# Kernel optimization log

Hardware: AMD Instinct MI355X
Metric: run time of the kernel (lower is better)

Reference implementation:

```python
import jax, jax.numpy as jnp
import numpy as np

D = 1024
H = 16
DH = D // H  # 64
FF_H = 4096
EPS = 1e-5


def layernorm(x, gamma, beta):
    mu = jnp.mean(x, axis=-1, keepdims=True)
    var = jnp.var(x, axis=-1, keepdims=True)
    return (x - mu) * jax.lax.rsqrt(var + EPS) * gamma + beta


def setup_inputs() -> dict:
    key = jax.random.key(0)
    ks = jax.random.split(key, 12)
    B, S = 2, 2048
    q = jax.random.normal(ks[0], (B, S, D), dtype=jnp.float32)
    k = jax.random.normal(ks[1], (B, S, D), dtype=jnp.float32)
    v = jax.random.normal(ks[2], (B, S, D), dtype=jnp.float32)
    time_lengths = jax.random.randint(ks[3], (B,), 0, S)
    mask = jnp.zeros((1, 1, S, S), dtype=jnp.float32)
    sc = 0.02
    Wq = jax.random.normal(ks[4], (D, D), dtype=jnp.float32) * sc
    Wk = jax.random.normal(ks[5], (D, D), dtype=jnp.float32) * sc
    Wv = jax.random.normal(ks[6], (D, D), dtype=jnp.float32) * sc
    Wd = jax.random.normal(ks[7], (D, D), dtype=jnp.float32) * sc
    W1 = jax.random.normal(ks[8], (D, FF_H), dtype=jnp.float32) * sc
    b1 = jnp.zeros((FF_H,), dtype=jnp.float32)
    W2 = jax.random.normal(ks[9], (FF_H, D), dtype=jnp.float32) * sc
    b2 = jnp.zeros((D,), dtype=jnp.float32)
    g1 = jnp.ones((D,), dtype=jnp.float32)
    be1 = jnp.zeros((D,), dtype=jnp.float32)
    g2 = jnp.ones((D,), dtype=jnp.float32)
    be2 = jnp.zeros((D,), dtype=jnp.float32)
    return {"q": q, "k": k, "v": v, "time_lengths": time_lengths, "mask": mask,
            "Wq": Wq, "Wk": Wk, "Wv": Wv, "Wd": Wd,
            "W1": W1, "b1": b1, "W2": W2, "b2": b2,
            "g1": g1, "be1": be1, "g2": g2, "be2": be2}


def reference(q, k, v, time_lengths, mask, Wq, Wk, Wv, Wd, W1, b1, W2, b2, g1, be1, g2, be2):
    B, S, _ = q.shape
    scale = jnp.sqrt(jnp.float32(DH))
    # project and split heads: [B,H,S,DH]
    qh = (q @ Wq).reshape(B, S, H, DH).transpose(0, 2, 1, 3)
    kh = (k @ Wk).reshape(B, S, H, DH).transpose(0, 2, 1, 3)
    vh = (v @ Wv).reshape(B, S, H, DH).transpose(0, 2, 1, 3)
    score = jnp.einsum('bhqd,bhkd->bhqk', qh, kh) / scale + mask
    attn = jax.nn.softmax(score, axis=-1)
    z = jnp.einsum('bhqk,bhkd->bhqd', attn, vh)
    z = z.transpose(0, 2, 1, 3).reshape(B, S, D)
    z = z @ Wd
    # Add & LayerNorm 1 (note: original applies LN to attn out, then adds q)
    x = layernorm(z, g1, be1) + q
    # FF (dropout is identity in eval)
    ff = jax.nn.relu(x @ W1 + b1) @ W2 + b2
    return layernorm(ff + x, g2, be2)
```

## Files before the change

### kernel.cpp

```cpp
#include <hip/hip_runtime.h>
#include <hip/hip_bf16.h>


#define SEQ 2048
#define DM  1024
#define LNEPS 1e-5f

typedef __attribute__((ext_vector_type(8))) short bf16x8;
typedef __attribute__((ext_vector_type(4))) float f32x4;

#define GAS __attribute__((address_space(1)))
#define LAS __attribute__((address_space(3)))

static __device__ __forceinline__ void gl_lds16(const unsigned short* g, unsigned short* l) {
    __builtin_amdgcn_global_load_lds((const GAS void*)g, (LAS void*)l, 16, 0, 0);
}

static __device__ __forceinline__ unsigned short f2bf(float f) {
    unsigned u = __builtin_bit_cast(unsigned, f);
    u += 0x7fffu + ((u >> 16) & 1u);
    return (unsigned short)(u >> 16);
}

__global__ __launch_bounds__(256) void gemm_bf16(
    const unsigned short* __restrict__ A, const unsigned short* __restrict__ Bt,
    float* __restrict__ Cf, unsigned short* __restrict__ Cb,
    int M, int N, int Klen, int lda, int ldb,
    size_t sA, size_t sB, size_t sC,
    const float* __restrict__ bias, int ep)
{
    __shared__ unsigned short As[128 * 32];
    __shared__ unsigned short Bs[128 * 32];

    const int t = threadIdx.x, lane = t & 63, w = t >> 6;
    const int wm = w >> 1, wn = w & 1;
    const int m0 = blockIdx.y * 128, n0 = blockIdx.x * 128;
    A  += (size_t)blockIdx.z * sA;
    Bt += (size_t)blockIdx.z * sB;
    const size_t cbase = (size_t)blockIdx.z * sC;
    const int l15 = lane & 15, l16 = lane >> 4;
    const int ar = lane >> 2, ac = (lane & 3) * 8;

    f32x4 acc[4][4];
    #pragma unroll
    for (int i = 0; i < 4; i++)
        #pragma unroll
        for (int j = 0; j < 4; j++)
            acc[i][j] = (f32x4){0.f, 0.f, 0.f, 0.f};

    for (int k0 = 0; k0 < Klen; k0 += 32) {
        __syncthreads();
        #pragma unroll
        for (int i = 0; i < 2; i++) {
            const int rg = w * 2 + i;
            gl_lds16(&A [(size_t)(m0 + rg * 16 + ar) * lda + k0 + ac], &As[rg * 512]);
            gl_lds16(&Bt[(size_t)(n0 + rg * 16 + ar) * ldb + k0 + ac], &Bs[rg * 512]);
        }
        __syncthreads();

        bf16x8 af[4], bfr[4];
        #pragma unroll
        for (int i = 0; i < 4; i++) {
            af[i]  = *(const bf16x8*)&As[(wm * 64 + i * 16 + l15) * 32 + l16 * 8];
            bfr[i] = *(const bf16x8*)&Bs[(wn * 64 + i * 16 + l15) * 32 + l16 * 8];
        }
        #pragma unroll
        for (int mi = 0; mi < 4; mi++)
            #pragma unroll
            for (int ni = 0; ni < 4; ni++)
                acc[mi][ni] = __builtin_amdgcn_mfma_f32_16x16x32_bf16(
                    af[mi], bfr[ni], acc[mi][ni], 0, 0, 0);
    }

    #pragma unroll
    for (int ni = 0; ni < 4; ni++) {
        const int col = n0 + wn * 64 + ni * 16 + l15;
        const float bv = (ep && blockIdx.z == 0) ? bias[col] : 0.f;
        #pragma unroll
        for (int mi = 0; mi < 4; mi++) {
            #pragma unroll
            for (int r = 0; r < 4; r++) {
                const int row = m0 + wm * 64 + mi * 16 + l16 * 4 + r;
                float vv = acc[mi][ni][r] + bv;
                if (ep == 2) vv = fmaxf(vv, 0.f);
                if (Cf) Cf[cbase + (size_t)row * N + col] = vv;
                else    Cb[cbase + (size_t)row * N + col] = f2bf(vv);
            }
        }
    }
}

__global__ __launch_bounds__(256) void attn_mfma(
    const unsigned short* __restrict__ qh, const unsigned short* __restrict__ kh,
    const unsigned short* __restrict__ vhT, const float* __restrict__ mask,
    unsigned short* __restrict__ z)
{
    __shared__ unsigned short Ks0[64 * 64];
    __shared__ unsigned short Ks1[64 * 64];
    __shared__ unsigned short Vst[64 * 64];
    __shared__ unsigned short Ps[64 * 72];

    const int t = threadIdx.x, lane = t & 63, w = t >> 6;
    const int bid = blockIdx.x;
    const int qt = bid >> 5, h = bid & 15, b = (bid >> 4) & 1;
    const int q0 = qt * 64, qr = w * 16;
    const int l15 = lane & 15, l16 = lane >> 4;

    const int lr = lane >> 3;
    const int gc = ((lane & 7) ^ lr) * 8;

    const size_t qbase = (size_t)(b * SEQ + q0) * DM + h * 64;
    const size_t kbase = (size_t)(b * SEQ) * DM + h * 64;
    const size_t vbase = (size_t)((b * 16 + h) * 64) * SEQ;

    #pragma unroll
    for (int i = 0; i < 2; i++) {
        const int rg = w * 2 + i;
        gl_lds16(&qh[qbase + (size_t)(rg * 8 + lr) * DM + gc], &Ks1[rg * 512]);
        gl_lds16(&kh[kbase + (size_t)(rg * 8 + lr) * DM + gc], &Ks0[rg * 512]);
    }
    __syncthreads();

    const int sw0 = ((l16    ) ^ (l15 & 7)) * 8;
    const int sw1 = ((l16 + 4) ^ (l15 & 7)) * 8;
    const bf16x8 bQ0 = *(const bf16x8*)&Ks1[(qr + l15) * 64 + sw0];
    const bf16x8 bQ1 = *(const bf16x8*)&Ks1[(qr + l15) * 64 + sw1];
    __syncthreads();

    const float* mrow = mask + (size_t)(q0 + qr + l15) * SEQ;

    float m_i = -1e30f, l_i = 0.f;
    f32x4 o4[4];
    #pragma unroll
    for (int mi = 0; mi < 4; mi++) o4[mi] = (f32x4){0.f, 0.f, 0.f, 0.f};

    for (int kt = 0; kt < SEQ / 64; kt++) {
        const int k0 = kt * 64;
        const int kn = ((kt + 1) & (SEQ / 64 - 1)) * 64;
        unsigned short* Kcur = (kt & 1) ? Ks1 : Ks0;
        unsigned short* Knxt = (kt & 1) ? Ks0 : Ks1;

        __builtin_amdgcn_s_barrier();

        float4 mv[4];
        #pragma unroll
        for (int ki = 0; ki < 4; ki++)
            mv[ki] = *(const float4*)&mrow[k0 + ki * 16 + l16 * 4];

        #pragma unroll
        for (int i = 0; i < 2; i++) {
            const int rg = w * 2 + i;
            gl_lds16(&vhT[vbase + (size_t)(rg * 8 + lr) * SEQ + k0 + gc], &Vst[rg * 512]);
        }
        __builtin_amdgcn_sched_barrier(0);
        #pragma unroll
        for (int i = 0; i < 2; i++) {
            const int rg = w * 2 + i;
            gl_lds16(&kh[kbase + (size_t)(kn + rg * 8 + lr) * DM + gc], &Knxt[rg * 512]);
        }

        asm volatile("s_waitcnt vmcnt(8)" ::: "memory");
        __builtin_amdgcn_s_barrier();
        __builtin_amdgcn_sched_barrier(0);

        f32x4 s4[4];
        __builtin_amdgcn_s_setprio(1);
        #pragma unroll
        for (int ki = 0; ki < 4; ki++) {
            const int r = ki * 16 + l15;
            const bf16x8 aK0 = *(const bf16x8*)&Kcur[r * 64 + sw0];
            const bf16x8 aK1 = *(const bf16x8*)&Kcur[r * 64 + sw1];
            f32x4 a0 = (f32x4){0.f, 0.f, 0.f, 0.f};
            a0 = __builtin_amdgcn_mfma_f32_16x16x32_bf16(aK0, bQ0, a0, 0, 0, 0);
            s4[ki] = __builtin_amdgcn_mfma_f32_16x16x32_bf16(aK1, bQ1, a0, 0, 0, 0);
        }
        __builtin_amdgcn_s_setprio(0);

        float sv[4][4];
        #pragma unroll
        for (int ki = 0; ki < 4; ki++) {
            sv[ki][0] = s4[ki][0] * 0.125f + mv[ki].x;
            sv[ki][1] = s4[ki][1] * 0.125f + mv[ki].y;
            sv[ki][2] = s4[ki][2] * 0.125f + mv[ki].z;
            sv[ki][3] = s4[ki][3] * 0.125f + mv[ki].w;
        }

        float rm = -1e30f;
        #pragma unroll
        for (int ki = 0; ki < 4; ki++)
            #pragma unroll
            for (int r = 0; r < 4; r++) rm = fmaxf(rm, sv[ki][r]);
        rm = fmaxf(rm, __shfl_xor(rm, 16));
        rm = fmaxf(rm, __shfl_xor(rm, 32));
        const float mnew  = fmaxf(m_i, rm);
        const float alpha = __expf(m_i - mnew);
        m_i = mnew;

        float ps = 0.f;
        #pragma unroll
        for (int ki = 0; ki < 4; ki++) {
            float p[4];
            #pragma unroll
            for (int r = 0; r < 4; r++) { p[r] = __expf(sv[ki][r] - mnew); ps += p[r]; }
            ushort4 pk;
            pk.x = f2bf(p[0]); pk.y = f2bf(p[1]); pk.z = f2bf(p[2]); pk.w = f2bf(p[3]);
            *(ushort4*)&Ps[(qr + l15) * 72 + ki * 16 + l16 * 4] = pk;
        }
        ps += __shfl_xor(ps, 16);
        ps += __shfl_xor(ps, 32);
        l_i = l_i * alpha + ps;
        #pragma unroll
        for (int mi = 0; mi < 4; mi++)
            #pragma unroll
            for (int r = 0; r < 4; r++) o4[mi][r] *= alpha;

        asm volatile("s_waitcnt vmcnt(2)" ::: "memory");
        __builtin_amdgcn_s_barrier();
        __builtin_amdgcn_sched_barrier(0);

        const bf16x8 bP0 = *(const bf16x8*)&Ps[(qr + l15) * 72 + l16 * 8];
        const bf16x8 bP1 = *(const bf16x8*)&Ps[(qr + l15) * 72 + 32 + l16 * 8];
        __builtin_amdgcn_s_setprio(1);
        #pragma unroll
        for (int mi = 0; mi < 4; mi++) {
            const int r = mi * 16 + l15;
            const bf16x8 aV0 = *(const bf16x8*)&Vst[r * 64 + sw0];
            const bf16x8 aV1 = *(const bf16x8*)&Vst[r * 64 + sw1];
            o4[mi] = __builtin_amdgcn_mfma_f32_16x16x32_bf16(aV0, bP0, o4[mi], 0, 0, 0);
            o4[mi] = __builtin_amdgcn_mfma_f32_16x16x32_bf16(aV1, bP1, o4[mi], 0, 0, 0);
        }
        __builtin_amdgcn_s_setprio(0);
    }

    asm volatile("s_waitcnt vmcnt(0)" ::: "memory");

    const float inv = 1.f / l_i;
    #pragma unroll
    for (int mi = 0; mi < 4; mi++) {
        ushort4 ok;
        ok.x = f2bf(o4[mi][0] * inv); ok.y = f2bf(o4[mi][1] * inv);
        ok.z = f2bf(o4[mi][2] * inv); ok.w = f2bf(o4[mi][3] * inv);
        *(ushort4*)&z[(size_t)(b * SEQ + q0 + qr + l15) * DM + h * 64 + mi * 16 + l16 * 4] = ok;
    }
}

__global__ __launch_bounds__(256) void cast3_bf16(
    const float* __restrict__ a0, const float* __restrict__ a1, const float* __restrict__ a2,
    unsigned short* __restrict__ out)
{
    const float* src = blockIdx.z == 0 ? a0 : (blockIdx.z == 1 ? a1 : a2);
    const size_t i = ((size_t)blockIdx.x * 256 + threadIdx.x) * 4;
    const float4 v = *(const float4*)&src[i];
    ushort4 o; o.x = f2bf(v.x); o.y = f2bf(v.y); o.z = f2bf(v.z); o.w = f2bf(v.w);
    *(ushort4*)&out[(size_t)blockIdx.z * ((size_t)SEQ * 2 * DM) + i] = o;
}

__global__ __launch_bounds__(256) void transpose_cast(
    const float* __restrict__ W, unsigned short* __restrict__ Wt, int K, int N)
{
    __shared__ float ts[64][65];
    const int n0 = blockIdx.x * 64, k0 = blockIdx.y * 64;
    const int t = threadIdx.x, r = t >> 4, c4 = (t & 15) * 4;
    #pragma unroll
    for (int i = 0; i < 4; i++) {
        const float4 v = *(const float4*)&W[(size_t)(k0 + r + i * 16) * N + n0 + c4];
        ts[r + i * 16][c4 + 0] = v.x; ts[r + i * 16][c4 + 1] = v.y;
        ts[r + i * 16][c4 + 2] = v.z; ts[r + i * 16][c4 + 3] = v.w;
    }
    __syncthreads();
    #pragma unroll
    for (int i = 0; i < 4; i++) {
        const int n = r + i * 16;
        ushort4 o;
        o.x = f2bf(ts[c4 + 0][n]); o.y = f2bf(ts[c4 + 1][n]);
        o.z = f2bf(ts[c4 + 2][n]); o.w = f2bf(ts[c4 + 3][n]);
        *(ushort4*)&Wt[(size_t)(n0 + n) * K + k0 + c4] = o;
    }
}

__global__ __launch_bounds__(256) void transpose_v(
    const unsigned short* __restrict__ vh, unsigned short* __restrict__ vhT)
{
    __shared__ unsigned short ts[64][80];
    const int s0 = blockIdx.x * 64, h = blockIdx.y, b = blockIdx.z;
    const int t = threadIdx.x, rr = t >> 3, c8 = (t & 7) * 8;
    #pragma unroll
    for (int i = 0; i < 2; i++) {
        const int srow = rr + i * 32;
        *(uint4*)&ts[srow][c8] = *(const uint4*)&vh[(size_t)(b * SEQ + s0 + srow) * DM + h * 64 + c8];
    }
    __syncthreads();
    #pragma unroll
    for (int i = 0; i < 2; i++) {
        const int dr = rr + i * 32;
        ushort4 ov0, ov1;
        ov0.x = ts[c8 + 0][dr]; ov0.y = ts[c8 + 1][dr];
        ov0.z = ts[c8 + 2][dr]; ov0.w = ts[c8 + 3][dr];
        ov1.x = ts[c8 + 4][dr]; ov1.y = ts[c8 + 5][dr];
        ov1.z = ts[c8 + 6][dr]; ov1.w = ts[c8 + 7][dr];
        *(ushort4*)&vhT[(size_t)((b * 16 + h) * 64 + dr) * SEQ + s0 + c8] = ov0;
        *(ushort4*)&vhT[(size_t)((b * 16 + h) * 64 + dr) * SEQ + s0 + c8 + 4] = ov1;
    }
}

__global__ __launch_bounds__(256) void ln_res(
    const float* __restrict__ a, const float* __restrict__ a2,
    const float* __restrict__ r,
    const float* __restrict__ g, const float* __restrict__ be,
    float* __restrict__ out, unsigned short* __restrict__ outb, int mode)
{
    __shared__ float redls[8];
    const int row = blockIdx.x, t = threadIdx.x;
    const size_t base = (size_t)row * DM;

    float vals[4], s = 0.f, sq = 0.f;
    #pragma unroll
    for (int i = 0; i < 4; i++) {
        const int c = t + 256 * i;
        float x = a[base + c];
        if (a2) x += a2[base + c];
        if (mode == 1) x += r[base + c];
        vals[i] = x; s += x; sq += x * x;
    }
    #pragma unroll
    for (int off = 32; off > 0; off >>= 1) { s += __shfl_down(s, off); sq += __shfl_down(sq, off); }
    if ((t & 63) == 0) { redls[t >> 6] = s; redls[4 + (t >> 6)] = sq; }
    __syncthreads();
    s  = redls[0] + redls[1] + redls[2] + redls[3];
    sq = redls[4] + redls[5] + redls[6] + redls[7];

    const float mu  = s * (1.f / 1024.f);
    const float var = sq * (1.f / 1024.f) - mu * mu;
    const float rs  = rsqrtf(var + LNEPS);
    #pragma unroll
    for (int i = 0; i < 4; i++) {
        const int c = t + 256 * i;
        float y = (vals[i] - mu) * rs * g[c] + be[c];
        if (mode == 0) y += r[base + c];
        out[base + c] = y;
        if (outb) outb[base + c] = f2bf(y);
    }
}

extern "C" void kernel_launch(void* const* d_in, const int* in_sizes, int n_in,
                              void* d_out, int out_size, void* d_ws, size_t ws_size,
                              hipStream_t stream)
{
    const float* q    = (const float*)d_in[0];
    const float* k    = (const float*)d_in[1];
    const float* v    = (const float*)d_in[2];
    const float* mask = (const float*)d_in[4];
    const float* Wq   = (const float*)d_in[5];
    const float* Wk   = (const float*)d_in[6];
    const float* Wv   = (const float*)d_in[7];
    const float* Wd   = (const float*)d_in[8];
    const float* W1   = (const float*)d_in[9];
    const float* b1   = (const float*)d_in[10];
    const float* W2   = (const float*)d_in[11];
    const float* b2   = (const float*)d_in[12];
    const float* g1   = (const float*)d_in[13];
    const float* be1  = (const float*)d_in[14];
    const float* g2   = (const float*)d_in[15];
    const float* be2  = (const float*)d_in[16];
    float* out = (float*)d_out;

    char* WS = (char*)d_ws;
    const size_t MiB = 1u << 20;
    const size_t ND  = (size_t)4096 * 1024;

    unsigned short* qb  = (unsigned short*)(WS + 0);
    unsigned short* vhT = (unsigned short*)(WS + 0);
    unsigned short* zb  = (unsigned short*)(WS + 8 * MiB);
    unsigned short* xb  = (unsigned short*)(WS + 16 * MiB);
    unsigned short* Wqt = (unsigned short*)(WS + 24 * MiB);
    unsigned short* Wdt = (unsigned short*)(WS + 30 * MiB);
    unsigned short* W1t = (unsigned short*)(WS + 32 * MiB);
    unsigned short* W2t = (unsigned short*)(WS + 40 * MiB);
    unsigned short* qh  = (unsigned short*)(WS + 48 * MiB);
    float*          zd0 = (float*)(WS + 48 * MiB);
    float*          zd1 = (float*)(WS + 64 * MiB);
    float*          x   = (float*)(WS + 80 * MiB);
    unsigned short* h1  = (unsigned short*)(WS + 96 * MiB);
    float*          y0  = (float*)(WS + 48 * MiB);
    float*          y1  = (float*)(WS + 64 * MiB);

    unsigned short* kh = qh + ND;
    unsigned short* vh = qh + 2 * ND;

    const dim3 blk(256);

    cast3_bf16<<<dim3(4096, 1, 3), blk, 0, stream>>>(q, k, v, qb);
    transpose_cast<<<dim3(16, 16), blk, 0, stream>>>(Wq, Wqt,                   1024, 1024);
    transpose_cast<<<dim3(16, 16), blk, 0, stream>>>(Wk, Wqt + 1024 * 1024,     1024, 1024);
    transpose_cast<<<dim3(16, 16), blk, 0, stream>>>(Wv, Wqt + 2 * 1024 * 1024, 1024, 1024);
    transpose_cast<<<dim3(16, 16), blk, 0, stream>>>(Wd, Wdt, 1024, 1024);
    transpose_cast<<<dim3(64, 16), blk, 0, stream>>>(W1, W1t, 1024, 4096);
    transpose_cast<<<dim3(16, 64), blk, 0, stream>>>(W2, W2t, 4096, 1024);

    gemm_bf16<<<dim3(8, 32, 3), blk, 0, stream>>>(qb, Wqt, nullptr, qh,
        4096, 1024, 1024, 1024, 1024, ND, (size_t)1024 * 1024, ND, nullptr, 0);

    transpose_v<<<dim3(32, 16, 2), blk, 0, stream>>>(vh, vhT);

    attn_mfma<<<dim3(1024), blk, 0, stream>>>(qh, kh, vhT, mask, zb);

    gemm_bf16<<<dim3(8, 32, 2), blk, 0, stream>>>(zb, Wdt, zd0, nullptr,
        4096, 1024, 512, 1024, 1024, 512, 512, ND, nullptr, 0);

    ln_res<<<dim3(4096), blk, 0, stream>>>(zd0, zd1, q, g1, be1, x, xb, 0);

    gemm_bf16<<<dim3(32, 32, 1), blk, 0, stream>>>(xb, W1t, nullptr, h1,
        4096, 4096, 1024, 1024, 1024, 0, 0, 0, b1, 2);
    gemm_bf16<<<dim3(8, 32, 2), blk, 0, stream>>>(h1, W2t, y0, nullptr,
        4096, 1024, 2048, 4096, 4096, 2048, 2048, ND, b2, 1);

    ln_res<<<dim3(4096), blk, 0, stream>>>(y0, y1, x, g2, be2, out, nullptr, 1);
}
```

Before: 495.8 us.

## Double-buffer GEMM, fuse V transpose into epilogue, merge prep kernels, lazy softmax rescale

```diff
diff --git a/kernel.cpp b/kernel.cpp
--- a/kernel.cpp
+++ b/kernel.cpp
@@ -22,15 +22,22 @@
     return (unsigned short)(u >> 16);
 }
 
+static __device__ __forceinline__ unsigned cvt_pk_bf16(float lo, float hi) {
+    unsigned r;
+    asm("v_cvt_pk_bf16_f32 %0, %1, %2" : "=v"(r) : "v"(lo), "v"(hi));
+    return r;
+}
+
 __global__ __launch_bounds__(256) void gemm_bf16(
     const unsigned short* __restrict__ A, const unsigned short* __restrict__ Bt,
     float* __restrict__ Cf, unsigned short* __restrict__ Cb,
+    unsigned short* __restrict__ CbT,
     int M, int N, int Klen, int lda, int ldb,
     size_t sA, size_t sB, size_t sC,
     const float* __restrict__ bias, int ep)
 {
-    __shared__ unsigned short As[128 * 32];
-    __shared__ unsigned short Bs[128 * 32];
+    __shared__ unsigned short As[2][128 * 32];
+    __shared__ unsigned short Bs[2][128 * 32];
 
     const int t = threadIdx.x, lane = t & 63, w = t >> 6;
     const int wm = w >> 1, wn = w & 1;
@@ -48,21 +55,20 @@
         for (int j = 0; j < 4; j++)
             acc[i][j] = (f32x4){0.f, 0.f, 0.f, 0.f};
 
-    for (int k0 = 0; k0 < Klen; k0 += 32) {
-        __syncthreads();
+    auto stage = [&](int buf, int k0) {
         #pragma unroll
         for (int i = 0; i < 2; i++) {
             const int rg = w * 2 + i;
-            gl_lds16(&A [(size_t)(m0 + rg * 16 + ar) * lda + k0 + ac], &As[rg * 512]);
-            gl_lds16(&Bt[(size_t)(n0 + rg * 16 + ar) * ldb + k0 + ac], &Bs[rg * 512]);
-        }
-        __syncthreads();
-
+            gl_lds16(&A [(size_t)(m0 + rg * 16 + ar) * lda + k0 + ac], &As[buf][rg * 512]);
+            gl_lds16(&Bt[(size_t)(n0 + rg * 16 + ar) * ldb + k0 + ac], &Bs[buf][rg * 512]);
+        }
+    };
+    auto compute = [&](int buf) {
         bf16x8 af[4], bfr[4];
         #pragma unroll
         for (int i = 0; i < 4; i++) {
-            af[i]  = *(const bf16x8*)&As[(wm * 64 + i * 16 + l15) * 32 + l16 * 8];
-            bfr[i] = *(const bf16x8*)&Bs[(wn * 64 + i * 16 + l15) * 32 + l16 * 8];
+            af[i]  = *(const bf16x8*)&As[buf][(wm * 64 + i * 16 + l15) * 32 + l16 * 8];
+            bfr[i] = *(const bf16x8*)&Bs[buf][(wn * 64 + i * 16 + l15) * 32 + l16 * 8];
         }
         #pragma unroll
         for (int mi = 0; mi < 4; mi++)
@@ -70,6 +76,35 @@
             for (int ni = 0; ni < 4; ni++)
                 acc[mi][ni] = __builtin_amdgcn_mfma_f32_16x16x32_bf16(
                     af[mi], bfr[ni], acc[mi][ni], 0, 0, 0);
+    };
+
+    stage(0, 0);
+    __syncthreads();
+    int k0 = 0;
+    for (; k0 + 32 < Klen; k0 += 32) {
+        const int cur = (k0 >> 5) & 1;
+        stage(cur ^ 1, k0 + 32);
+        compute(cur);
+        __syncthreads();
+    }
+    compute((k0 >> 5) & 1);
+
+    if (CbT && blockIdx.z == 2) {
+        #pragma unroll
+        for (int ni = 0; ni < 4; ni++) {
+            const int col = n0 + wn * 64 + ni * 16 + l15;
+            const int hh = col >> 6, d = col & 63;
+            #pragma unroll
+            for (int mi = 0; mi < 4; mi++) {
+                const int row = m0 + wm * 64 + mi * 16 + l16 * 4;
+                const int bb = row >> 11, s = row & 2047;
+                ushort4 o;
+                o.x = f2bf(acc[mi][ni][0]); o.y = f2bf(acc[mi][ni][1]);
+                o.z = f2bf(acc[mi][ni][2]); o.w = f2bf(acc[mi][ni][3]);
+                *(ushort4*)&CbT[((size_t)((bb * 16 + hh) * 64 + d)) * SEQ + s] = o;
+            }
+        }
+        return;
     }
 
     #pragma unroll
@@ -176,43 +211,50 @@
         }
         __builtin_amdgcn_s_setprio(0);
 
-        float sv[4][4];
+        float sv[16];
         #pragma unroll
         for (int ki = 0; ki < 4; ki++) {
-            sv[ki][0] = s4[ki][0] * 0.125f + mv[ki].x;
-            sv[ki][1] = s4[ki][1] * 0.125f + mv[ki].y;
-            sv[ki][2] = s4[ki][2] * 0.125f + mv[ki].z;
-            sv[ki][3] = s4[ki][3] * 0.125f + mv[ki].w;
-        }
-
-        float rm = -1e30f;
-        #pragma unroll
-        for (int ki = 0; ki < 4; ki++)
-            #pragma unroll
-            for (int r = 0; r < 4; r++) rm = fmaxf(rm, sv[ki][r]);
+            sv[ki * 4 + 0] = s4[ki][0] * 0.125f + mv[ki].x;
+            sv[ki * 4 + 1] = s4[ki][1] * 0.125f + mv[ki].y;
+            sv[ki * 4 + 2] = s4[ki][2] * 0.125f + mv[ki].z;
+            sv[ki * 4 + 3] = s4[ki][3] * 0.125f + mv[ki].w;
+        }
+
+        float rm = fmaxf(sv[0], sv[1]);
+        #pragma unroll
+        for (int i = 2; i < 16; i += 2) rm = fmaxf(fmaxf(rm, sv[i]), sv[i + 1]);
         rm = fmaxf(rm, __shfl_xor(rm, 16));
         rm = fmaxf(rm, __shfl_xor(rm, 32));
-        const float mnew  = fmaxf(m_i, rm);
-        const float alpha = __expf(m_i - mnew);
-        m_i = mnew;
+
+        const bool skip = __all(rm <= m_i + 8.f);
+        float mnew = m_i, alpha = 1.f;
+        if (!skip) { mnew = fmaxf(m_i, rm); alpha = __expf(m_i - mnew); }
 
         float ps = 0.f;
         #pragma unroll
         for (int ki = 0; ki < 4; ki++) {
-            float p[4];
-            #pragma unroll
-            for (int r = 0; r < 4; r++) { p[r] = __expf(sv[ki][r] - mnew); ps += p[r]; }
-            ushort4 pk;
-            pk.x = f2bf(p[0]); pk.y = f2bf(p[1]); pk.z = f2bf(p[2]); pk.w = f2bf(p[3]);
-            *(ushort4*)&Ps[(qr + l15) * 72 + ki * 16 + l16 * 4] = pk;
+            const float p0 = __expf(sv[ki * 4 + 0] - mnew);
+            const float p1 = __expf(sv[ki * 4 + 1] - mnew);
+            const float p2 = __expf(sv[ki * 4 + 2] - mnew);
+            const float p3 = __expf(sv[ki * 4 + 3] - mnew);
+            ps += (p0 + p1) + (p2 + p3);
+            uint2 pk;
+            pk.x = cvt_pk_bf16(p0, p1);
+            pk.y = cvt_pk_bf16(p2, p3);
+            *(uint2*)&Ps[(qr + l15) * 72 + ki * 16 + l16 * 4] = pk;
         }
         ps += __shfl_xor(ps, 16);
         ps += __shfl_xor(ps, 32);
-        l_i = l_i * alpha + ps;
-        #pragma unroll
-        for (int mi = 0; mi < 4; mi++)
+        if (!skip) {
+            m_i = mnew;
+            l_i = l_i * alpha + ps;
             #pragma unroll
-            for (int r = 0; r < 4; r++) o4[mi][r] *= alpha;
+            for (int mi = 0; mi < 4; mi++)
+                #pragma unroll
+                for (int r = 0; r < 4; r++) o4[mi][r] *= alpha;
+        } else {
+            l_i += ps;
+        }
 
         asm volatile("s_waitcnt vmcnt(2)" ::: "memory");
         __builtin_amdgcn_s_barrier();
@@ -237,35 +279,63 @@
     const float inv = 1.f / l_i;
     #pragma unroll
     for (int mi = 0; mi < 4; mi++) {
-        ushort4 ok;
-        ok.x = f2bf(o4[mi][0] * inv); ok.y = f2bf(o4[mi][1] * inv);
-        ok.z = f2bf(o4[mi][2] * inv); ok.w = f2bf(o4[mi][3] * inv);
-        *(ushort4*)&z[(size_t)(b * SEQ + q0 + qr + l15) * DM + h * 64 + mi * 16 + l16 * 4] = ok;
-    }
-}
-
-__global__ __launch_bounds__(256) void cast3_bf16(
-    const float* __restrict__ a0, const float* __restrict__ a1, const float* __restrict__ a2,
-    unsigned short* __restrict__ out)
+        const float a0 = o4[mi][0] * inv, a1 = o4[mi][1] * inv;
+        const float a2 = o4[mi][2] * inv, a3 = o4[mi][3] * inv;
+        uint2 ov;
+        ov.x = cvt_pk_bf16(a0, a1);
+        ov.y = cvt_pk_bf16(a2, a3);
+        *(uint2*)&z[(size_t)(b * SEQ + q0 + qr + l15) * DM + h * 64 + mi * 16 + l16 * 4] = ov;
+    }
+}
+
+__global__ __launch_bounds__(256) void prep(
+    const float* __restrict__ q, const float* __restrict__ k, const float* __restrict__ v,
+    unsigned short* __restrict__ qb,
+    const float* __restrict__ Wq, const float* __restrict__ Wk,
+    const float* __restrict__ Wv, const float* __restrict__ Wd,
+    const float* __restrict__ W1, const float* __restrict__ W2,
+    unsigned short* __restrict__ Wqt, unsigned short* __restrict__ Wdt,
+    unsigned short* __restrict__ W1t, unsigned short* __restrict__ W2t)
 {
-    const float* src = blockIdx.z == 0 ? a0 : (blockIdx.z == 1 ? a1 : a2);
-    const size_t i = ((size_t)blockIdx.x * 256 + threadIdx.x) * 4;
-    const float4 v = *(const float4*)&src[i];
-    ushort4 o; o.x = f2bf(v.x); o.y = f2bf(v.y); o.z = f2bf(v.z); o.w = f2bf(v.w);
-    *(ushort4*)&out[(size_t)blockIdx.z * ((size_t)SEQ * 2 * DM) + i] = o;
-}
-
-__global__ __launch_bounds__(256) void transpose_cast(
-    const float* __restrict__ W, unsigned short* __restrict__ Wt, int K, int N)
-{
+    const int z = blockIdx.z, t = threadIdx.x;
+    const int flat = blockIdx.y * 64 + blockIdx.x;
+
+    if (z < 3) {
+        const float* src = z == 0 ? q : (z == 1 ? k : v);
+        unsigned short* dst = qb + (size_t)z * ((size_t)SEQ * 2 * DM);
+        const size_t base = (size_t)flat * 4096 + t * 4;
+        #pragma unroll
+        for (int i = 0; i < 4; i++) {
+            const float4 w4 = *(const float4*)&src[base + i * 1024];
+            ushort4 o; o.x = f2bf(w4.x); o.y = f2bf(w4.y); o.z = f2bf(w4.z); o.w = f2bf(w4.w);
+            *(ushort4*)&dst[base + i * 1024] = o;
+        }
+        return;
+    }
+
     __shared__ float ts[64][65];
-    const int n0 = blockIdx.x * 64, k0 = blockIdx.y * 64;
-    const int t = threadIdx.x, r = t >> 4, c4 = (t & 15) * 4;
+    const float* W; unsigned short* Wt; int K, N, n0, k0;
+    if (z < 7) {
+        if (flat >= 256) return;
+        W  = z == 3 ? Wq : z == 4 ? Wk : (z == 5 ? Wv : Wd);
+        Wt = z == 3 ? Wqt : z == 4 ? Wqt + 1024 * 1024
+           : z == 5 ? Wqt + 2 * 1024 * 1024 : Wdt;
+        K = 1024; N = 1024;
+        n0 = (flat & 15) * 64; k0 = (flat >> 4) * 64;
+    } else if (z == 7) {
+        W = W1; Wt = W1t; K = 1024; N = 4096;
+        n0 = blockIdx.x * 64; k0 = blockIdx.y * 64;
+    } else {
+        W = W2; Wt = W2t; K = 4096; N = 1024;
+        n0 = (flat & 15) * 64; k0 = (flat >> 4) * 64;
+    }
+
+    const int r = t >> 4, c4 = (t & 15) * 4;
     #pragma unroll
     for (int i = 0; i < 4; i++) {
-        const float4 v = *(const float4*)&W[(size_t)(k0 + r + i * 16) * N + n0 + c4];
-        ts[r + i * 16][c4 + 0] = v.x; ts[r + i * 16][c4 + 1] = v.y;
-        ts[r + i * 16][c4 + 2] = v.z; ts[r + i * 16][c4 + 3] = v.w;
+        const float4 v4 = *(const float4*)&W[(size_t)(k0 + r + i * 16) * N + n0 + c4];
+        ts[r + i * 16][c4 + 0] = v4.x; ts[r + i * 16][c4 + 1] = v4.y;
+        ts[r + i * 16][c4 + 2] = v4.z; ts[r + i * 16][c4 + 3] = v4.w;
     }
     __syncthreads();
     #pragma unroll
@@ -275,31 +345,6 @@
         o.x = f2bf(ts[c4 + 0][n]); o.y = f2bf(ts[c4 + 1][n]);
         o.z = f2bf(ts[c4 + 2][n]); o.w = f2bf(ts[c4 + 3][n]);
         *(ushort4*)&Wt[(size_t)(n0 + n) * K + k0 + c4] = o;
-    }
-}
-
-__global__ __launch_bounds__(256) void transpose_v(
-    const unsigned short* __restrict__ vh, unsigned short* __restrict__ vhT)
-{
-    __shared__ unsigned short ts[64][80];
-    const int s0 = blockIdx.x * 64, h = blockIdx.y, b = blockIdx.z;
-    const int t = threadIdx.x, rr = t >> 3, c8 = (t & 7) * 8;
-    #pragma unroll
-    for (int i = 0; i < 2; i++) {
-        const int srow = rr + i * 32;
-        *(uint4*)&ts[srow][c8] = *(const uint4*)&vh[(size_t)(b * SEQ + s0 + srow) * DM + h * 64 + c8];
-    }
-    __syncthreads();
-    #pragma unroll
-    for (int i = 0; i < 2; i++) {
-        const int dr = rr + i * 32;
-        ushort4 ov0, ov1;
-        ov0.x = ts[c8 + 0][dr]; ov0.y = ts[c8 + 1][dr];
-        ov0.z = ts[c8 + 2][dr]; ov0.w = ts[c8 + 3][dr];
-        ov1.x = ts[c8 + 4][dr]; ov1.y = ts[c8 + 5][dr];
-        ov1.z = ts[c8 + 6][dr]; ov1.w = ts[c8 + 7][dr];
-        *(ushort4*)&vhT[(size_t)((b * 16 + h) * 64 + dr) * SEQ + s0 + c8] = ov0;
-        *(ushort4*)&vhT[(size_t)((b * 16 + h) * 64 + dr) * SEQ + s0 + c8 + 4] = ov1;
     }
 }
 
@@ -369,7 +414,6 @@
     const size_t ND  = (size_t)4096 * 1024;
 
     unsigned short* qb  = (unsigned short*)(WS + 0);
-    unsigned short* vhT = (unsigned short*)(WS + 0);
     unsigned short* zb  = (unsigned short*)(WS + 8 * MiB);
     unsigned short* xb  = (unsigned short*)(WS + 16 * MiB);
     unsigned short* Wqt = (unsigned short*)(WS + 24 * MiB);
@@ -377,6 +421,7 @@
     unsigned short* W1t = (unsigned short*)(WS + 32 * MiB);
     unsigned short* W2t = (unsigned short*)(WS + 40 * MiB);
     unsigned short* qh  = (unsigned short*)(WS + 48 * MiB);
+    unsigned short* vhT = (unsigned short*)(WS + 64 * MiB);
     float*          zd0 = (float*)(WS + 48 * MiB);
     float*          zd1 = (float*)(WS + 64 * MiB);
     float*          x   = (float*)(WS + 80 * MiB);
@@ -385,33 +430,25 @@
     float*          y1  = (float*)(WS + 64 * MiB);
 
     unsigned short* kh = qh + ND;
-    unsigned short* vh = qh + 2 * ND;
 
     const dim3 blk(256);
 
-    cast3_bf16<<<dim3(4096, 1, 3), blk, 0, stream>>>(q, k, v, qb);
-    transpose_cast<<<dim3(16, 16), blk, 0, stream>>>(Wq, Wqt,                   1024, 1024);
-    transpose_cast<<<dim3(16, 16), blk, 0, stream>>>(Wk, Wqt + 1024 * 1024,     1024, 1024);
-    transpose_cast<<<dim3(16, 16), blk, 0, stream>>>(Wv, Wqt + 2 * 1024 * 1024, 1024, 1024);
-    transpose_cast<<<dim3(16, 16), blk, 0, stream>>>(Wd, Wdt, 1024, 1024);
-    transpose_cast<<<dim3(64, 16), blk, 0, stream>>>(W1, W1t, 1024, 4096);
-    transpose_cast<<<dim3(16, 64), blk, 0, stream>>>(W2, W2t, 4096, 1024);
-
-    gemm_bf16<<<dim3(8, 32, 3), blk, 0, stream>>>(qb, Wqt, nullptr, qh,
+    prep<<<dim3(64, 16, 9), blk, 0, stream>>>(q, k, v, qb, Wq, Wk, Wv, Wd, W1, W2,
+                                              Wqt, Wdt, W1t, W2t);
+
+    gemm_bf16<<<dim3(8, 32, 3), blk, 0, stream>>>(qb, Wqt, nullptr, qh, vhT,
         4096, 1024, 1024, 1024, 1024, ND, (size_t)1024 * 1024, ND, nullptr, 0);
 
-    transpose_v<<<dim3(32, 16, 2), blk, 0, stream>>>(vh, vhT);
-
     attn_mfma<<<dim3(1024), blk, 0, stream>>>(qh, kh, vhT, mask, zb);
 
-    gemm_bf16<<<dim3(8, 32, 2), blk, 0, stream>>>(zb, Wdt, zd0, nullptr,
+    gemm_bf16<<<dim3(8, 32, 2), blk, 0, stream>>>(zb, Wdt, zd0, nullptr, nullptr,
         4096, 1024, 512, 1024, 1024, 512, 512, ND, nullptr, 0);
 
     ln_res<<<dim3(4096), blk, 0, stream>>>(zd0, zd1, q, g1, be1, x, xb, 0);
 
-    gemm_bf16<<<dim3(32, 32, 1), blk, 0, stream>>>(xb, W1t, nullptr, h1,
+    gemm_bf16<<<dim3(32, 32, 1), blk, 0, stream>>>(xb, W1t, nullptr, h1, nullptr,
         4096, 4096, 1024, 1024, 1024, 0, 0, 0, b1, 2);
-    gemm_bf16<<<dim3(8, 32, 2), blk, 0, stream>>>(h1, W2t, y0, nullptr,
+    gemm_bf16<<<dim3(8, 32, 2), blk, 0, stream>>>(h1, W2t, y0, nullptr, nullptr,
         4096, 1024, 2048, 4096, 4096, 2048, 2048, ND, b2, 1);
 
     ln_res<<<dim3(4096), blk, 0, stream>>>(y0, y1, x, g2, be2, out, nullptr, 1);
```

Measured after the change: 477.3 us. 3.7% less time.
